# Optimization experiments

Measured on AMD Instinct MI355X. Metric: run time of the kernel, lower is better.

Reference implementation:

```python
import jax, jax.numpy as jnp
import numpy as np

NUM_HEADS = 16
D_MODEL = 1024
DEPTH = D_MODEL // NUM_HEADS


def rope_sincos(seq_len, depth):
    # standard RoPE: inv_freq over even dims, sin/cos tiled to full depth
    inv_freq = 1.0 / (10000.0 ** (jnp.arange(0, depth, 2, dtype=jnp.float32) / depth))
    ang = jnp.arange(seq_len, dtype=jnp.float32)[:, None] * inv_freq[None, :]  # [S, depth/2]
    sin = jnp.concatenate([jnp.sin(ang), jnp.sin(ang)], axis=-1)  # [S, depth]
    cos = jnp.concatenate([jnp.cos(ang), jnp.cos(ang)], axis=-1)
    return sin, cos


def apply_rope(x, sin, cos):
    # x: [B,H,S,depth]; rotate-half formulation
    half = x.shape[-1] // 2
    x1, x2 = x[..., :half], x[..., half:]
    rot = jnp.concatenate([-x2, x1], axis=-1)
    return x * cos + rot * sin


def setup_inputs() -> dict:
    key = jax.random.key(0)
    ks = jax.random.split(key, 5)
    s = 1.0 / np.sqrt(D_MODEL)
    return {
        "x": jax.random.normal(ks[0], (2, 2048, D_MODEL), dtype=jnp.float32),
        "wq": jax.random.normal(ks[1], (D_MODEL, D_MODEL), dtype=jnp.float32) * s,
        "bq": jnp.zeros((D_MODEL,), jnp.float32),
        "wk": jax.random.normal(ks[2], (D_MODEL, D_MODEL), dtype=jnp.float32) * s,
        "bk": jnp.zeros((D_MODEL,), jnp.float32),
        "wv": jax.random.normal(ks[3], (D_MODEL, D_MODEL), dtype=jnp.float32) * s,
        "bv": jnp.zeros((D_MODEL,), jnp.float32),
        "wo": jax.random.normal(ks[4], (D_MODEL, D_MODEL), dtype=jnp.float32) * s,
        "bo": jnp.zeros((D_MODEL,), jnp.float32),
    }


def reference(x, wq, bq, wk, bk, wv, bv, wo, bo):
    B, S, _ = x.shape

    def split_heads(t):  # [B,S,D] -> [B,H,S,depth]
        return t.reshape(B, S, NUM_HEADS, DEPTH).transpose(0, 2, 1, 3)

    Q = split_heads(x @ wq + bq)
    K = split_heads(x @ wk + bk)
    V = split_heads(x @ wv + bv)

    sin, cos = rope_sincos(S, DEPTH)  # [S, depth], broadcasts over B,H
    Q = apply_rope(Q, sin, cos)
    K = apply_rope(K, sin, cos)

    scores = jnp.einsum("bhqd,bhkd->bhqk", Q, K) / jnp.sqrt(jnp.float32(DEPTH))
    weights = jax.nn.softmax(scores, axis=-1)
    out = jnp.einsum("bhqk,bhkd->bhqd", weights, V)
    out = out.transpose(0, 2, 1, 3).reshape(B, S, D_MODEL)
    return out @ wo + bo
```

## Files before the change

### kernel.cpp

```cpp
#include <hip/hip_runtime.h>

#define DM 1024
#define SEQ 2048
#define NH 16
#define DH 64
#define BATCH 2

typedef _Float16 half_t;
typedef _Float16 half8 __attribute__((ext_vector_type(8)));
typedef _Float16 half4 __attribute__((ext_vector_type(4)));
typedef __fp16 f16x2 __attribute__((ext_vector_type(2)));
typedef unsigned u32x2 __attribute__((ext_vector_type(2)));
typedef float f32x4 __attribute__((ext_vector_type(4)));

__device__ __forceinline__ f32x4 mfma16(half8 a, half8 b, f32x4 c) {
  return __builtin_amdgcn_mfma_f32_16x16x32_f16(a, b, c, 0, 0, 0);
}

__device__ __forceinline__ void gl2lds16(const half_t* g, half_t* l) {
  __builtin_amdgcn_global_load_lds((const __attribute__((address_space(1))) void*)g,
                                   (__attribute__((address_space(3))) void*)l, 16, 0, 0);
}


__global__ void cvt_x_kernel(const float* __restrict__ x, half_t* __restrict__ xh) {
  int i = (blockIdx.x * 256 + threadIdx.x) * 4;
  float4 v = *(const float4*)(x + i);
  half4 h = { (half_t)v.x, (half_t)v.y, (half_t)v.z, (half_t)v.w };
  *(half4*)(xh + i) = h;
}

__global__ void wtrans_kernel(const float* __restrict__ w0, const float* __restrict__ w1,
                              const float* __restrict__ w2, const float* __restrict__ w3,
                              half_t* __restrict__ o0, half_t* __restrict__ o1,
                              half_t* __restrict__ o2, half_t* __restrict__ o3) {
  __shared__ float tile[32][33];
  const float* w = (blockIdx.z == 0) ? w0 : (blockIdx.z == 1) ? w1 : (blockIdx.z == 2) ? w2 : w3;
  half_t* o = (blockIdx.z == 0) ? o0 : (blockIdx.z == 1) ? o1 : (blockIdx.z == 2) ? o2 : o3;
  int tx = threadIdx.x, ty0 = threadIdx.y;
  int bx = blockIdx.x * 32, by = blockIdx.y * 32;
#pragma unroll
  for (int i = 0; i < 4; i++) {
    int ty = ty0 + i * 8;
    tile[ty][tx] = w[(size_t)(by + ty) * DM + bx + tx];
  }
  __syncthreads();
#pragma unroll
  for (int i = 0; i < 4; i++) {
    int ty = ty0 + i * 8;
    o[(size_t)(bx + ty) * DM + by + tx] = (half_t)tile[tx][ty];
  }
}

__global__ void ropetab_kernel(float* __restrict__ st, float* __restrict__ ct) {
  int idx = blockIdx.x * 256 + threadIdx.x;
  int s = idx >> 5, i = idx & 31;
  float freq = exp2f(-(float)i * (13.287712379549449f / 32.0f));
  float ang = (float)s * freq;
  st[idx] = sinf(ang);
  ct[idx] = cosf(ang);
}

__global__ __launch_bounds__(256)
void vtrans_kernel(const half_t* __restrict__ Vh, half_t* __restrict__ Vt) {
  __shared__ half_t t[64 * 72];
  const int tid = threadIdx.x;
  const int bh = blockIdx.y;
  const int s0 = blockIdx.x * 64;
  const half_t* src = Vh + (size_t)bh * SEQ * DH + (size_t)s0 * DH;
  half_t* dst = Vt + (size_t)bh * DH * SEQ;
#pragma unroll
  for (int i = 0; i < 2; i++) {
    int s = tid + i * 256;
    int row = s >> 3, blk = s & 7;
    *(half8*)&t[row * 72 + blk * 8] = *(const half8*)&src[(size_t)row * DH + blk * 8];
  }
  __syncthreads();
  const int d = tid >> 2;
#pragma unroll
  for (int i = 0; i < 2; i++) {
    int sb = (tid & 3) * 8 + i * 32;
    half8 v;
#pragma unroll
    for (int j = 0; j < 8; j++) v[j] = t[(sb + j) * 72 + d];
    *(half8*)&dst[(size_t)d * SEQ + s0 + sb] = v;
  }
}


__global__ __launch_bounds__(256)
void qkv_kernel(const half_t* __restrict__ xh,
                const half_t* __restrict__ wtq, const half_t* __restrict__ wtk,
                const half_t* __restrict__ wtv,
                const float* __restrict__ bq, const float* __restrict__ bk,
                const float* __restrict__ bv,
                const float* __restrict__ st, const float* __restrict__ ctab,
                half_t* __restrict__ Qh, half_t* __restrict__ Kh, half_t* __restrict__ Vh) {
  const int tid = threadIdx.x;
  const int wid = tid >> 6, lane = tid & 63;
  const int l16 = lane & 15, quad = lane >> 4;
  const int m0 = blockIdx.y * 128, n0 = blockIdx.x * 128;
  const int g = blockIdx.z;
  const half_t* wt = (g == 0) ? wtq : (g == 1) ? wtk : wtv;
  const float* bias = (g == 0) ? bq : (g == 1) ? bk : bv;
  __shared__ __align__(16) half_t As[128 * 32];
  __shared__ __align__(16) half_t Bs[128 * 32];
  f32x4 acc[4][4] = {};
  const int wrow = (wid >> 1) * 64, wcol = (wid & 1) * 64;

  const int ar0 = tid >> 2,          ab0 = (tid & 3) ^ ((ar0 >> 1) & 3);
  const int ar1 = (tid + 256) >> 2,  ab1 = (tid & 3) ^ ((ar1 >> 1) & 3);
  const int swz = (l16 >> 1) & 3;

  for (int k0 = 0; k0 < DM; k0 += 32) {
    __syncthreads();
    gl2lds16(&xh[(size_t)(m0 + ar0) * DM + k0 + ab0 * 8], &As[tid * 8]);
    gl2lds16(&xh[(size_t)(m0 + ar1) * DM + k0 + ab1 * 8], &As[(tid + 256) * 8]);
    gl2lds16(&wt[(size_t)(n0 + ar0) * DM + k0 + ab0 * 8], &Bs[tid * 8]);
    gl2lds16(&wt[(size_t)(n0 + ar1) * DM + k0 + ab1 * 8], &Bs[(tid + 256) * 8]);
    __syncthreads();
    half8 a[4], b[4];
#pragma unroll
    for (int rt = 0; rt < 4; rt++)
      a[rt] = *(const half8*)&As[((wrow + rt * 16 + l16) * 4 + (quad ^ swz)) * 8];
#pragma unroll
    for (int ct = 0; ct < 4; ct++)
      b[ct] = *(const half8*)&Bs[((wcol + ct * 16 + l16) * 4 + (quad ^ swz)) * 8];
#pragma unroll
    for (int rt = 0; rt < 4; rt++)
#pragma unroll
      for (int ct = 0; ct < 4; ct++)
        acc[rt][ct] = mfma16(a[rt], b[ct], acc[rt][ct]);
  }

  const int h = (n0 + wcol) >> 6;
  const float qscale = 0.125f * 1.44269504089f;
  half_t* dst = (g == 0) ? Qh : (g == 1) ? Kh : Vh;
  float bv4[4];
#pragma unroll
  for (int ct = 0; ct < 4; ct++) bv4[ct] = bias[n0 + wcol + ct * 16 + l16];
#pragma unroll
  for (int rt = 0; rt < 4; rt++) {
#pragma unroll
    for (int r = 0; r < 4; r++) {
      int m = m0 + wrow + rt * 16 + quad * 4 + r;
      int bb = m >> 11, s = m & 2047;
      float v0 = acc[rt][0][r] + bv4[0];
      float v1 = acc[rt][1][r] + bv4[1];
      float v2 = acc[rt][2][r] + bv4[2];
      float v3 = acc[rt][3][r] + bv4[3];
      float o0 = v0, o1 = v1, o2 = v2, o3 = v3;
      if (g != 2) {
        float sn0 = st[s * 32 + l16], cs0 = ctab[s * 32 + l16];
        float sn1 = st[s * 32 + 16 + l16], cs1 = ctab[s * 32 + 16 + l16];
        o0 = v0 * cs0 - v2 * sn0;
        o1 = v1 * cs1 - v3 * sn1;
        o2 = v2 * cs0 + v0 * sn0;
        o3 = v3 * cs1 + v1 * sn1;
        if (g == 0) { o0 *= qscale; o1 *= qscale; o2 *= qscale; o3 *= qscale; }
      }
      size_t base = ((size_t)(bb * NH + h) * SEQ + s) * DH;
      dst[base + l16]      = (half_t)o0;
      dst[base + 16 + l16] = (half_t)o1;
      dst[base + 32 + l16] = (half_t)o2;
      dst[base + 48 + l16] = (half_t)o3;
    }
  }
}


__global__ __launch_bounds__(256)
void attn_kernel(const half_t* __restrict__ Qh, const half_t* __restrict__ Kh,
                 const half_t* __restrict__ Vt, half_t* __restrict__ AO) {
  const int tid = threadIdx.x;
  const int wid = tid >> 6, lane = tid & 63;
  const int l16 = lane & 15, quad = lane >> 4;
  const int bh = blockIdx.y;
  const int bb = bh >> 4, h = bh & 15;
  const int q0 = blockIdx.x * 128 + wid * 32;
  const half_t* Q = Qh + (size_t)bh * SEQ * DH;
  const half_t* K = Kh + (size_t)bh * SEQ * DH;
  const half_t* V = Vt + (size_t)bh * DH * SEQ;
  __shared__ __align__(16) half_t Ks[2][64 * 64];
  __shared__ __align__(16) half_t Vs[2][64 * 64];
  __shared__ __align__(16) half_t pbuf[4][32 * 72];
  half_t* myp = pbuf[wid];

  const int r0 = tid >> 3,         c0 = (tid & 7) ^ (r0 & 7);
  const int r1 = (tid + 256) >> 3, c1 = (tid & 7) ^ (r1 & 7);
  const int sw0 = ((quad ^ (l16 & 7)) * 8);
  const int sw1 = (((quad + 4) ^ (l16 & 7)) * 8);

  half8 aqA[2], aqB[2];
#pragma unroll
  for (int rt = 0; rt < 2; rt++) {
    aqA[rt] = *(const half8*)&Q[(size_t)(q0 + rt * 16 + l16) * DH + quad * 8];
    aqB[rt] = *(const half8*)&Q[(size_t)(q0 + rt * 16 + l16) * DH + 32 + quad * 8];
  }

  f32x4 o[2][4] = {};
  f32x4 vsum[2] = {};
  const f32x4 cinit = {-12.f, -12.f, -12.f, -12.f};

  gl2lds16(&K[(size_t)r0 * DH + c0 * 8], &Ks[0][tid * 8]);
  gl2lds16(&K[(size_t)r1 * DH + c1 * 8], &Ks[0][(tid + 256) * 8]);
  gl2lds16(&V[(size_t)r0 * SEQ + c0 * 8], &Vs[0][tid * 8]);
  gl2lds16(&V[(size_t)r1 * SEQ + c1 * 8], &Vs[0][(tid + 256) * 8]);
  __syncthreads();

  int cur = 0;
  for (int kb0 = 0; kb0 < SEQ; kb0 += 64) {
    const int nxt = cur ^ 1;
    if (kb0 + 64 < SEQ) {
      const int kb = kb0 + 64;
      gl2lds16(&K[(size_t)(kb + r0) * DH + c0 * 8], &Ks[nxt][tid * 8]);
      gl2lds16(&K[(size_t)(kb + r1) * DH + c1 * 8], &Ks[nxt][(tid + 256) * 8]);
      gl2lds16(&V[(size_t)r0 * SEQ + kb + c0 * 8], &Vs[nxt][tid * 8]);
      gl2lds16(&V[(size_t)r1 * SEQ + kb + c1 * 8], &Vs[nxt][(tid + 256) * 8]);
    }
    const half_t* ksrc = Ks[cur];
    const half_t* vsrc = Vs[cur];

    f32x4 z[2][4];
    __builtin_amdgcn_s_setprio(1);
#pragma unroll
    for (int kt = 0; kt < 4; kt++) {
      const half_t* krow = &ksrc[(kt * 16 + l16) * 64];
      half8 b0 = *(const half8*)&krow[sw0];
      half8 b1 = *(const half8*)&krow[sw1];
#pragma unroll
      for (int rt = 0; rt < 2; rt++) {
        f32x4 zz = cinit;
        zz = mfma16(b0, aqA[rt], zz);
        zz = mfma16(b1, aqB[rt], zz);
        z[rt][kt] = zz;
      }
    }
    __builtin_amdgcn_s_setprio(0);

#pragma unroll
    for (int rt = 0; rt < 2; rt++)
#pragma unroll
      for (int kt = 0; kt < 4; kt++) {
        f32x4 p;
#pragma unroll
        for (int r = 0; r < 4; r++) p[r] = __builtin_amdgcn_exp2f(z[rt][kt][r]);
        vsum[rt] += p;
        f16x2 lo = __builtin_amdgcn_cvt_pkrtz(p[0], p[1]);
        f16x2 hi = __builtin_amdgcn_cvt_pkrtz(p[2], p[3]);
        u32x2 w = { __builtin_bit_cast(unsigned, lo), __builtin_bit_cast(unsigned, hi) };
        *(u32x2*)&myp[(rt * 16 + l16) * 72 + kt * 16 + quad * 4] = w;
      }

    half8 ap0[2], ap1[2];
#pragma unroll
    for (int rt = 0; rt < 2; rt++) {
      ap0[rt] = *(const half8*)&myp[(rt * 16 + l16) * 72 + quad * 8];
      ap1[rt] = *(const half8*)&myp[(rt * 16 + l16) * 72 + 32 + quad * 8];
    }
    __builtin_amdgcn_s_setprio(1);
#pragma unroll
    for (int dt = 0; dt < 4; dt++) {
      const half_t* vrow = &vsrc[(dt * 16 + l16) * 64];
      half8 bv0 = *(const half8*)&vrow[sw0];
      half8 bv1 = *(const half8*)&vrow[sw1];
#pragma unroll
      for (int rt = 0; rt < 2; rt++) {
        o[rt][dt] = mfma16(ap0[rt], bv0, o[rt][dt]);
        o[rt][dt] = mfma16(ap1[rt], bv1, o[rt][dt]);
      }
    }
    __builtin_amdgcn_s_setprio(0);

    __syncthreads();
    cur = nxt;
  }

  float linv[2][4];
#pragma unroll
  for (int rt = 0; rt < 2; rt++) {
    float s = (vsum[rt][0] + vsum[rt][1]) + (vsum[rt][2] + vsum[rt][3]);
    s += __shfl_xor(s, 16);
    s += __shfl_xor(s, 32);
#pragma unroll
    for (int r = 0; r < 4; r++) linv[rt][r] = 1.f / __shfl(s, quad * 4 + r);
  }
#pragma unroll
  for (int rt = 0; rt < 2; rt++)
#pragma unroll
    for (int dt = 0; dt < 4; dt++)
#pragma unroll
      for (int r = 0; r < 4; r++) {
        int srow = q0 + rt * 16 + quad * 4 + r;
        AO[((size_t)bb * SEQ + srow) * DM + h * DH + dt * 16 + l16] =
            (half_t)(o[rt][dt][r] * linv[rt][r]);
      }
}


__global__ __launch_bounds__(256)
void out_kernel(const half_t* __restrict__ AO, const half_t* __restrict__ wto,
                const float* __restrict__ bo, float* __restrict__ out) {
  const int tid = threadIdx.x;
  const int wid = tid >> 6, lane = tid & 63;
  const int l16 = lane & 15, quad = lane >> 4;
  const int m0 = blockIdx.y * 128, n0 = blockIdx.x * 64;
  __shared__ __align__(16) half_t As[128 * 32];
  __shared__ __align__(16) half_t Bs[64 * 32];
  f32x4 acc[4][2] = {};
  const int wrow = (wid >> 1) * 64, wcol = (wid & 1) * 32;

  const int ar0 = tid >> 2,         ab0 = (tid & 3) ^ ((ar0 >> 1) & 3);
  const int ar1 = (tid + 256) >> 2, ab1 = (tid & 3) ^ ((ar1 >> 1) & 3);
  const int swz = (l16 >> 1) & 3;

  for (int k0 = 0; k0 < DM; k0 += 32) {
    __syncthreads();
    gl2lds16(&AO[(size_t)(m0 + ar0) * DM + k0 + ab0 * 8], &As[tid * 8]);
    gl2lds16(&AO[(size_t)(m0 + ar1) * DM + k0 + ab1 * 8], &As[(tid + 256) * 8]);
    gl2lds16(&wto[(size_t)(n0 + ar0) * DM + k0 + ab0 * 8], &Bs[tid * 8]);
    __syncthreads();
    half8 a[4], b[2];
#pragma unroll
    for (int rt = 0; rt < 4; rt++)
      a[rt] = *(const half8*)&As[((wrow + rt * 16 + l16) * 4 + (quad ^ swz)) * 8];
#pragma unroll
    for (int ct = 0; ct < 2; ct++)
      b[ct] = *(const half8*)&Bs[((wcol + ct * 16 + l16) * 4 + (quad ^ swz)) * 8];
#pragma unroll
    for (int rt = 0; rt < 4; rt++)
#pragma unroll
      for (int ct = 0; ct < 2; ct++)
        acc[rt][ct] = mfma16(a[rt], b[ct], acc[rt][ct]);
  }
  float bv2[2];
#pragma unroll
  for (int ct = 0; ct < 2; ct++) bv2[ct] = bo[n0 + wcol + ct * 16 + l16];
#pragma unroll
  for (int rt = 0; rt < 4; rt++)
#pragma unroll
    for (int r = 0; r < 4; r++) {
      int m = m0 + wrow + rt * 16 + quad * 4 + r;
#pragma unroll
      for (int ct = 0; ct < 2; ct++)
        out[(size_t)m * DM + n0 + wcol + ct * 16 + l16] = acc[rt][ct][r] + bv2[ct];
    }
}


extern "C" void kernel_launch(void* const* d_in, const int* in_sizes, int n_in,
                              void* d_out, int out_size, void* d_ws, size_t ws_size,
                              hipStream_t stream) {
  (void)in_sizes; (void)n_in; (void)out_size; (void)ws_size;
  const float* x  = (const float*)d_in[0];
  const float* wq = (const float*)d_in[1];
  const float* bq = (const float*)d_in[2];
  const float* wk = (const float*)d_in[3];
  const float* bk = (const float*)d_in[4];
  const float* wv = (const float*)d_in[5];
  const float* bv = (const float*)d_in[6];
  const float* wo = (const float*)d_in[7];
  const float* bo = (const float*)d_in[8];
  char* ws = (char*)d_ws;
  const size_t MB = 1u << 20;
  half_t* xh  = (half_t*)(ws + 0);
  half_t* AO  = (half_t*)(ws + 0);
  half_t* wtq = (half_t*)(ws + 8 * MB);
  half_t* wtk = (half_t*)(ws + 10 * MB);
  half_t* wtv = (half_t*)(ws + 12 * MB);
  half_t* wto = (half_t*)(ws + 14 * MB);
  float*  st  = (float*)(ws + 16 * MB);
  float*  ctb = (float*)(ws + 16 * MB + 256 * 1024);
  half_t* Qh  = (half_t*)(ws + 17 * MB);
  half_t* Kh  = (half_t*)(ws + 25 * MB);
  half_t* Vh  = (half_t*)(ws + 33 * MB);
  half_t* Vt  = (half_t*)(ws + 41 * MB);
  float* out = (float*)d_out;

  cvt_x_kernel<<<4096, 256, 0, stream>>>(x, xh);
  wtrans_kernel<<<dim3(32, 32, 4), dim3(32, 8), 0, stream>>>(wq, wk, wv, wo, wtq, wtk, wtv, wto);
  ropetab_kernel<<<256, 256, 0, stream>>>(st, ctb);
  qkv_kernel<<<dim3(8, 32, 3), 256, 0, stream>>>(xh, wtq, wtk, wtv, bq, bk, bv, st, ctb, Qh, Kh, Vh);
  vtrans_kernel<<<dim3(32, 32), 256, 0, stream>>>(Vh, Vt);
  attn_kernel<<<dim3(16, 32), 256, 0, stream>>>(Qh, Kh, Vt, AO);
  out_kernel<<<dim3(16, 32), 256, 0, stream>>>(AO, wto, bo, out);
}
```

Before: 204.9 us.

## Fuse V transpose into QKV epilogue and register-stage attention K/V prefetch

The V projection's epilogue now writes a transposed [d, seq] layout via a per-wave LDS tile, so the separate vtrans kernel and its extra HBM pass over V are removed. In the attention loop, next-block K/V tiles are loaded into registers at the start of the iteration and stored to LDS after compute, replacing the direct global-to-LDS loads. The extra 36KB LDS tile in the QKV kernel may reduce occupancy for all blocks, and register staging raises register pressure in attention.

```diff
diff --git a/kernel.cpp b/kernel.cpp
--- a/kernel.cpp
+++ b/kernel.cpp
@@ -11,6 +11,7 @@
 typedef _Float16 half4 __attribute__((ext_vector_type(4)));
 typedef __fp16 f16x2 __attribute__((ext_vector_type(2)));
 typedef unsigned u32x2 __attribute__((ext_vector_type(2)));
+typedef unsigned u32x4 __attribute__((ext_vector_type(4)));
 typedef float f32x4 __attribute__((ext_vector_type(4)));
 
 __device__ __forceinline__ f32x4 mfma16(half8 a, half8 b, f32x4 c) {
@@ -61,32 +62,6 @@
   ct[idx] = cosf(ang);
 }
 
-__global__ __launch_bounds__(256)
-void vtrans_kernel(const half_t* __restrict__ Vh, half_t* __restrict__ Vt) {
-  __shared__ half_t t[64 * 72];
-  const int tid = threadIdx.x;
-  const int bh = blockIdx.y;
-  const int s0 = blockIdx.x * 64;
-  const half_t* src = Vh + (size_t)bh * SEQ * DH + (size_t)s0 * DH;
-  half_t* dst = Vt + (size_t)bh * DH * SEQ;
-#pragma unroll
-  for (int i = 0; i < 2; i++) {
-    int s = tid + i * 256;
-    int row = s >> 3, blk = s & 7;
-    *(half8*)&t[row * 72 + blk * 8] = *(const half8*)&src[(size_t)row * DH + blk * 8];
-  }
-  __syncthreads();
-  const int d = tid >> 2;
-#pragma unroll
-  for (int i = 0; i < 2; i++) {
-    int sb = (tid & 3) * 8 + i * 32;
-    half8 v;
-#pragma unroll
-    for (int j = 0; j < 8; j++) v[j] = t[(sb + j) * 72 + d];
-    *(half8*)&dst[(size_t)d * SEQ + s0 + sb] = v;
-  }
-}
-
 
 __global__ __launch_bounds__(256)
 void qkv_kernel(const half_t* __restrict__ xh,
@@ -95,7 +70,7 @@
                 const float* __restrict__ bq, const float* __restrict__ bk,
                 const float* __restrict__ bv,
                 const float* __restrict__ st, const float* __restrict__ ctab,
-                half_t* __restrict__ Qh, half_t* __restrict__ Kh, half_t* __restrict__ Vh) {
+                half_t* __restrict__ Qh, half_t* __restrict__ Kh, half_t* __restrict__ Vt) {
   const int tid = threadIdx.x;
   const int wid = tid >> 6, lane = tid & 63;
   const int l16 = lane & 15, quad = lane >> 4;
@@ -105,6 +80,7 @@
   const float* bias = (g == 0) ? bq : (g == 1) ? bk : bv;
   __shared__ __align__(16) half_t As[128 * 32];
   __shared__ __align__(16) half_t Bs[128 * 32];
+  __shared__ __align__(16) half_t vtile[4][64 * 72];
   f32x4 acc[4][4] = {};
   const int wrow = (wid >> 1) * 64, wcol = (wid & 1) * 64;
 
@@ -135,35 +111,55 @@
 
   const int h = (n0 + wcol) >> 6;
   const float qscale = 0.125f * 1.44269504089f;
-  half_t* dst = (g == 0) ? Qh : (g == 1) ? Kh : Vh;
   float bv4[4];
 #pragma unroll
   for (int ct = 0; ct < 4; ct++) bv4[ct] = bias[n0 + wcol + ct * 16 + l16];
-#pragma unroll
-  for (int rt = 0; rt < 4; rt++) {
-#pragma unroll
-    for (int r = 0; r < 4; r++) {
-      int m = m0 + wrow + rt * 16 + quad * 4 + r;
-      int bb = m >> 11, s = m & 2047;
-      float v0 = acc[rt][0][r] + bv4[0];
-      float v1 = acc[rt][1][r] + bv4[1];
-      float v2 = acc[rt][2][r] + bv4[2];
-      float v3 = acc[rt][3][r] + bv4[3];
-      float o0 = v0, o1 = v1, o2 = v2, o3 = v3;
-      if (g != 2) {
+
+  if (g == 2) {
+    half_t* vt = vtile[wid];
+#pragma unroll
+    for (int rt = 0; rt < 4; rt++)
+#pragma unroll
+      for (int ct = 0; ct < 4; ct++) {
+        half4 hv;
+#pragma unroll
+        for (int r = 0; r < 4; r++) hv[r] = (half_t)(acc[rt][ct][r] + bv4[ct]);
+        *(half4*)&vt[(ct * 16 + l16) * 72 + rt * 16 + quad * 4] = hv;
+      }
+    const int sb = m0 + wrow;
+    const int bb = sb >> 11, s0 = sb & 2047;
+    half_t* dstv = Vt + (size_t)(bb * NH + h) * DH * SEQ;
+#pragma unroll
+    for (int i = 0; i < 8; i++) {
+      int d = i * 8 + (lane >> 3), soff = (lane & 7) * 8;
+      half8 v = *(const half8*)&vt[d * 72 + soff];
+      *(half8*)&dstv[(size_t)d * SEQ + s0 + soff] = v;
+    }
+  } else {
+    half_t* dst = (g == 0) ? Qh : Kh;
+#pragma unroll
+    for (int rt = 0; rt < 4; rt++) {
+#pragma unroll
+      for (int r = 0; r < 4; r++) {
+        int m = m0 + wrow + rt * 16 + quad * 4 + r;
+        int bb = m >> 11, s = m & 2047;
+        float v0 = acc[rt][0][r] + bv4[0];
+        float v1 = acc[rt][1][r] + bv4[1];
+        float v2 = acc[rt][2][r] + bv4[2];
+        float v3 = acc[rt][3][r] + bv4[3];
         float sn0 = st[s * 32 + l16], cs0 = ctab[s * 32 + l16];
         float sn1 = st[s * 32 + 16 + l16], cs1 = ctab[s * 32 + 16 + l16];
-        o0 = v0 * cs0 - v2 * sn0;
-        o1 = v1 * cs1 - v3 * sn1;
-        o2 = v2 * cs0 + v0 * sn0;
-        o3 = v3 * cs1 + v1 * sn1;
+        float o0 = v0 * cs0 - v2 * sn0;
+        float o1 = v1 * cs1 - v3 * sn1;
+        float o2 = v2 * cs0 + v0 * sn0;
+        float o3 = v3 * cs1 + v1 * sn1;
         if (g == 0) { o0 *= qscale; o1 *= qscale; o2 *= qscale; o3 *= qscale; }
-      }
-      size_t base = ((size_t)(bb * NH + h) * SEQ + s) * DH;
-      dst[base + l16]      = (half_t)o0;
-      dst[base + 16 + l16] = (half_t)o1;
-      dst[base + 32 + l16] = (half_t)o2;
-      dst[base + 48 + l16] = (half_t)o3;
+        size_t base = ((size_t)(bb * NH + h) * SEQ + s) * DH;
+        dst[base + l16]      = (half_t)o0;
+        dst[base + 16 + l16] = (half_t)o1;
+        dst[base + 32 + l16] = (half_t)o2;
+        dst[base + 48 + l16] = (half_t)o3;
+      }
     }
   }
 }
@@ -191,6 +187,11 @@
   const int sw0 = ((quad ^ (l16 & 7)) * 8);
   const int sw1 = (((quad + 4) ^ (l16 & 7)) * 8);
 
+  const half_t* gK0 = &K[(size_t)r0 * DH + c0 * 8];
+  const half_t* gK1 = &K[(size_t)r1 * DH + c1 * 8];
+  const half_t* gV0 = &V[(size_t)r0 * SEQ + c0 * 8];
+  const half_t* gV1 = &V[(size_t)r1 * SEQ + c1 * 8];
+
   half8 aqA[2], aqB[2];
 #pragma unroll
   for (int rt = 0; rt < 2; rt++) {
@@ -202,21 +203,22 @@
   f32x4 vsum[2] = {};
   const f32x4 cinit = {-12.f, -12.f, -12.f, -12.f};
 
-  gl2lds16(&K[(size_t)r0 * DH + c0 * 8], &Ks[0][tid * 8]);
-  gl2lds16(&K[(size_t)r1 * DH + c1 * 8], &Ks[0][(tid + 256) * 8]);
-  gl2lds16(&V[(size_t)r0 * SEQ + c0 * 8], &Vs[0][tid * 8]);
-  gl2lds16(&V[(size_t)r1 * SEQ + c1 * 8], &Vs[0][(tid + 256) * 8]);
+  gl2lds16(gK0, &Ks[0][tid * 8]);
+  gl2lds16(gK1, &Ks[0][(tid + 256) * 8]);
+  gl2lds16(gV0, &Vs[0][tid * 8]);
+  gl2lds16(gV1, &Vs[0][(tid + 256) * 8]);
   __syncthreads();
 
   int cur = 0;
   for (int kb0 = 0; kb0 < SEQ; kb0 += 64) {
-    const int nxt = cur ^ 1;
-    if (kb0 + 64 < SEQ) {
+    const bool pf = (kb0 + 64 < SEQ);
+    u32x4 rk0, rk1, rv0, rv1;
+    if (pf) {
       const int kb = kb0 + 64;
-      gl2lds16(&K[(size_t)(kb + r0) * DH + c0 * 8], &Ks[nxt][tid * 8]);
-      gl2lds16(&K[(size_t)(kb + r1) * DH + c1 * 8], &Ks[nxt][(tid + 256) * 8]);
-      gl2lds16(&V[(size_t)r0 * SEQ + kb + c0 * 8], &Vs[nxt][tid * 8]);
-      gl2lds16(&V[(size_t)r1 * SEQ + kb + c1 * 8], &Vs[nxt][(tid + 256) * 8]);
+      rk0 = *(const u32x4*)(gK0 + (size_t)kb * DH);
+      rk1 = *(const u32x4*)(gK1 + (size_t)kb * DH);
+      rv0 = *(const u32x4*)(gV0 + kb);
+      rv1 = *(const u32x4*)(gV1 + kb);
     }
     const half_t* ksrc = Ks[cur];
     const half_t* vsrc = Vs[cur];
@@ -272,8 +274,15 @@
     }
     __builtin_amdgcn_s_setprio(0);
 
-    __syncthreads();
-    cur = nxt;
+    if (pf) {
+      const int nxt = cur ^ 1;
+      *(u32x4*)&Ks[nxt][tid * 8] = rk0;
+      *(u32x4*)&Ks[nxt][(tid + 256) * 8] = rk1;
+      *(u32x4*)&Vs[nxt][tid * 8] = rv0;
+      *(u32x4*)&Vs[nxt][(tid + 256) * 8] = rv1;
+    }
+    __syncthreads();
+    cur ^= 1;
   }
 
   float linv[2][4];
@@ -373,15 +382,13 @@
   float*  ctb = (float*)(ws + 16 * MB + 256 * 1024);
   half_t* Qh  = (half_t*)(ws + 17 * MB);
   half_t* Kh  = (half_t*)(ws + 25 * MB);
-  half_t* Vh  = (half_t*)(ws + 33 * MB);
-  half_t* Vt  = (half_t*)(ws + 41 * MB);
+  half_t* Vt  = (half_t*)(ws + 33 * MB);
   float* out = (float*)d_out;
 
   cvt_x_kernel<<<4096, 256, 0, stream>>>(x, xh);
   wtrans_kernel<<<dim3(32, 32, 4), dim3(32, 8), 0, stream>>>(wq, wk, wv, wo, wtq, wtk, wtv, wto);
   ropetab_kernel<<<256, 256, 0, stream>>>(st, ctb);
-  qkv_kernel<<<dim3(8, 32, 3), 256, 0, stream>>>(xh, wtq, wtk, wtv, bq, bk, bv, st, ctb, Qh, Kh, Vh);
-  vtrans_kernel<<<dim3(32, 32), 256, 0, stream>>>(Vh, Vt);
+  qkv_kernel<<<dim3(8, 32, 3), 256, 0, stream>>>(xh, wtq, wtk, wtv, bq, bk, bv, st, ctb, Qh, Kh, Vt);
   attn_kernel<<<dim3(16, 32), 256, 0, stream>>>(Qh, Kh, Vt, AO);
   out_kernel<<<dim3(16, 32), 256, 0, stream>>>(AO, wto, bo, out);
 }
```

Result: no change. 207.5 us (+1.2%).
